# Optimization experiments

Measured on AMD Instinct MI355X. Metric: run time of the kernel, lower is better.

## Reference

```python
import jax, jax.numpy as jnp
import numpy as np

N_NODES = 100000
N_EDGES = 1600000


def setup_inputs() -> dict:
    key = jax.random.key(0)
    k1, k2, k3, k4, k5, k6 = jax.random.split(key, 6)
    x = jax.random.normal(k1, (N_NODES, 2), dtype=jnp.float32)
    edge_index = jax.random.randint(k2, (2, N_EDGES), 0, N_NODES, dtype=jnp.int64)
    # Glorot-style init for GCN weights, zeros for biases (PyG defaults)
    W1 = jax.random.normal(k3, (2, 64), dtype=jnp.float32) * (1.0 / np.sqrt(2.0))
    b1 = jnp.zeros((64,), dtype=jnp.float32)
    W2 = jax.random.normal(k4, (64, 1), dtype=jnp.float32) * (1.0 / np.sqrt(64.0))
    b2 = jnp.zeros((1,), dtype=jnp.float32)
    return {"x": x, "edge_index": edge_index, "W1": W1, "b1": b1, "W2": W2, "b2": b2}


def reference(x, edge_index, W1, b1, W2, b2):
    N = x.shape[0]
    row, col = edge_index[0], edge_index[1]  # source, target (PyG flow source_to_target)
    # symmetric GCN normalization, degrees from target index (no self loops)
    deg = jax.ops.segment_sum(jnp.ones(edge_index.shape[1], x.dtype), col, num_segments=N)
    deg_inv_sqrt = jnp.where(deg > 0, jnp.where(deg > 0, deg, 1.0) ** -0.5, 0.0)
    norm = (deg_inv_sqrt[row] * deg_inv_sqrt[col])[:, None]  # [E,1]

    def gcn_conv(h, W, b):
        h = h @ W                       # [N,F_out] tiny GEMM
        msg = h[row] * norm             # gather + scale: [E,F_out]
        agg = jax.ops.segment_sum(msg, col, num_segments=N)  # scatter-add
        return agg + b

    h = jax.nn.relu(gcn_conv(x, W1, b1))   # dropout is identity in eval mode
    out = jax.nn.relu(gcn_conv(h, W2, b2))
    return out
```

## Files before the change

### kernel.cpp

```cpp
#include <hip/hip_runtime.h>
#include <math.h>

#define NN 100000
#define NE 1600000
#define BKT 448
#define NB 224
#define EPB 6400
#define NPB 250
#define STRIDE 8192
#define RT 1024

__global__ void __launch_bounds__(RT) reorder_kernel(
        const int* __restrict__ row, const int* __restrict__ col,
        unsigned* __restrict__ cursor, unsigned* __restrict__ packed) {
    __shared__ int h[NB], lb[NB];
    __shared__ unsigned gaddr[NB], glim[NB];
    __shared__ int wsum[RT / 64];
    __shared__ uint2 sga[EPB];
    const int t = threadIdx.x;
    const int lane = t & 63, wid = t >> 6;
    const int e0 = blockIdx.x * EPB;

    for (int i = t; i < NB; i += RT) h[i] = 0;
    __syncthreads();

    const int4* rv = (const int4*)(row + e0);
    const int4* cv = (const int4*)(col + e0);
    unsigned pk[8]; int bb[8];
#pragma unroll
    for (int u = 0; u < 8; ++u) bb[u] = -1;
#pragma unroll
    for (int g = 0; g < 2; ++g) {
        int grp = g * RT + t;
        if (grp < EPB / 4) {
            int4 r4 = rv[grp], c4 = cv[grp];
            int rr[4] = {r4.x, r4.y, r4.z, r4.w};
            int cc[4] = {c4.x, c4.y, c4.z, c4.w};
#pragma unroll
            for (int j = 0; j < 4; ++j) {
                int b = cc[j] / BKT;
                int cl = cc[j] - b * BKT;
                pk[4 * g + j] = ((unsigned)rr[j] << 9) | (unsigned)cl;
                bb[4 * g + j] = b;
            }
        }
    }
#pragma unroll
    for (int u = 0; u < 8; ++u)
        if (bb[u] >= 0) atomicAdd(&h[bb[u]], 1);
    __syncthreads();

    int v = (t < NB) ? h[t] : 0;
    int incl = v;
#pragma unroll
    for (int d = 1; d < 64; d <<= 1) {
        int u2 = __shfl_up(incl, d);
        if (lane >= d) incl += u2;
    }
    if (lane == 63) wsum[wid] = incl;
    __syncthreads();
    int off = 0;
#pragma unroll
    for (int j = 0; j < 3; ++j)
        if (j < wid) off += wsum[j];
    if (t < NB) {
        lb[t] = off + incl - v;
        unsigned base = v ? atomicAdd(&cursor[t], (unsigned)v) : 0u;
        gaddr[t] = (unsigned)t * STRIDE + base;
        glim[t]  = (unsigned)(t + 1) * STRIDE;
    }
    __syncthreads();
    for (int i = t; i < NB; i += RT) h[i] = 0;
    __syncthreads();

#pragma unroll
    for (int u = 0; u < 8; ++u) {
        if (bb[u] >= 0) {
            int b = bb[u];
            int r = atomicAdd(&h[b], 1);
            unsigned a = gaddr[b] + (unsigned)r;
            if (a >= glim[b]) a = 0xFFFFFFFFu;
            sga[lb[b] + r] = make_uint2(pk[u], a);
        }
    }
    __syncthreads();
    for (int i = t; i < EPB; i += RT) {
        uint2 e = sga[i];
        if (e.y != 0xFFFFFFFFu) packed[e.y] = e.x;
    }
}

__global__ void __launch_bounds__(RT) sortb_kernel(
        const unsigned* __restrict__ packed, const unsigned* __restrict__ cursor,
        const float2* __restrict__ x2,
        unsigned* __restrict__ srow, int2* __restrict__ node_rng,
        float* __restrict__ dis, float2* __restrict__ y2) {
    __shared__ int cnt[BKT], rk[BKT], sexA[BKT];
    __shared__ int wsum[(BKT + 63) / 64];
    __shared__ unsigned srt[STRIDE];
    const int t = threadIdx.x;
    const int lane = t & 63, wid = t >> 6;
    const int b = blockIdx.x;
    const unsigned s0 = (unsigned)b * STRIDE;
    const int L = min((int)cursor[b], STRIDE);
    const int L4 = L >> 2;

    for (int i = t; i < BKT; i += RT) { cnt[i] = 0; rk[i] = 0; }
    __syncthreads();

    const uint4* pv4 = (const uint4*)(packed + s0);
    for (int g = t; g < L4; g += RT) {
        uint4 p4 = pv4[g];
        atomicAdd(&cnt[p4.x & 511u], 1);
        atomicAdd(&cnt[p4.y & 511u], 1);
        atomicAdd(&cnt[p4.z & 511u], 1);
        atomicAdd(&cnt[p4.w & 511u], 1);
    }
    for (int i = 4 * L4 + t; i < L; i += RT)
        atomicAdd(&cnt[packed[s0 + i] & 511u], 1);
    __syncthreads();

    int v = (t < BKT) ? cnt[t] : 0;
    int incl = v;
#pragma unroll
    for (int d = 1; d < 64; d <<= 1) {
        int u2 = __shfl_up(incl, d);
        if (lane >= d) incl += u2;
    }
    if (lane == 63 && wid < (BKT + 63) / 64) wsum[wid] = incl;
    __syncthreads();
    int off = 0;
#pragma unroll
    for (int j = 0; j < (BKT + 63) / 64 - 1; ++j)
        if (j < wid) off += wsum[j];
    if (t < BKT) {
        int sex = off + incl - v;
        sexA[t] = sex;
        int node = b * BKT + t;
        if (node < NN) {
            float dv = (v > 0) ? rsqrtf((float)v) : 0.0f;
            dis[node] = dv;
            float2 xv = x2[node];
            y2[node] = make_float2(xv.x * dv, xv.y * dv);
            node_rng[node] = make_int2((int)(s0 + sex), (int)(s0 + sex + v));
        }
    }
    __syncthreads();

    for (int g = t; g < L4; g += RT) {
        uint4 p4 = pv4[g];
        unsigned pp[4] = {p4.x, p4.y, p4.z, p4.w};
#pragma unroll
        for (int j = 0; j < 4; ++j) {
            int cl = pp[j] & 511u;
            int r = atomicAdd(&rk[cl], 1);
            srt[sexA[cl] + r] = pp[j] >> 9;
        }
    }
    for (int i = 4 * L4 + t; i < L; i += RT) {
        unsigned p = packed[s0 + i];
        int cl = p & 511u;
        int r = atomicAdd(&rk[cl], 1);
        srt[sexA[cl] + r] = p >> 9;
    }
    __syncthreads();
    uint4* so4 = (uint4*)(srow + s0);
    for (int g = t; g < L4; g += RT) so4[g] = ((const uint4*)srt)[g];
    for (int i = 4 * L4 + t; i < L; i += RT) srow[s0 + i] = srt[i];
}

__global__ void conv1_kernel(const unsigned* __restrict__ srow, const int2* __restrict__ node_rng,
                             const float2* __restrict__ y2, const float* __restrict__ dis,
                             const float* __restrict__ W1, const float* __restrict__ b1,
                             const float* __restrict__ W2, float* __restrict__ z2) {
    __shared__ float sW0[64], sW1[64], sb1[64], sW2[64];
    int t = threadIdx.x;
    if (t < 64) { sW0[t] = W1[t]; sW1[t] = W1[64 + t]; sb1[t] = b1[t]; sW2[t] = W2[t]; }
    __syncthreads();
    int lane = t & 3;
    int node = blockIdx.x * 64 + (t >> 2);
    if (node >= NN) return;
    int2 rng = node_rng[node];
    float sx = 0.f, sy = 0.f;
    for (int k = rng.x + lane; k < rng.y; k += 4) {
        float2 v = y2[srow[k]];
        sx += v.x; sy += v.y;
    }
    sx += __shfl_xor(sx, 1); sy += __shfl_xor(sy, 1);
    sx += __shfl_xor(sx, 2); sy += __shfl_xor(sy, 2);
    float dv = dis[node];
    float a0 = sx * dv, a1 = sy * dv;
    float acc = 0.0f;
    int j0 = lane * 16;
#pragma unroll
    for (int jj = 0; jj < 16; ++jj) {
        int j = j0 + jj;
        float h = fmaf(a0, sW0[j], fmaf(a1, sW1[j], sb1[j]));
        acc = fmaf(fmaxf(h, 0.0f), sW2[j], acc);
    }
    acc += __shfl_xor(acc, 1);
    acc += __shfl_xor(acc, 2);
    if (lane == 0) z2[node] = acc * dv;
}

__global__ void conv2_kernel(const unsigned* __restrict__ srow, const int2* __restrict__ node_rng,
                             const float* __restrict__ z2, const float* __restrict__ dis,
                             const float* __restrict__ b2, float* __restrict__ out) {
    int t = threadIdx.x;
    int lane = t & 3;
    int node = blockIdx.x * 64 + (t >> 2);
    if (node >= NN) return;
    int2 rng = node_rng[node];
    float s = 0.f;
    for (int k = rng.x + lane; k < rng.y; k += 4)
        s += z2[srow[k]];
    s += __shfl_xor(s, 1);
    s += __shfl_xor(s, 2);
    if (lane == 0)
        out[node] = fmaxf(fmaf(dis[node], s, b2[0]), 0.0f);
}

extern "C" void kernel_launch(void* const* d_in, const int* in_sizes, int n_in,
                              void* d_out, int out_size, void* d_ws, size_t ws_size,
                              hipStream_t stream) {
    const float* x  = (const float*)d_in[0];
    const int*   ei = (const int*)d_in[1];
    const float* W1 = (const float*)d_in[2];
    const float* b1 = (const float*)d_in[3];
    const float* W2 = (const float*)d_in[4];
    const float* b2 = (const float*)d_in[5];
    float* out = (float*)d_out;

    const int* row = ei;
    const int* col = ei + NE;

    unsigned* packed   = (unsigned*)d_ws;
    unsigned* srow     = packed + (size_t)NB * STRIDE;
    float2*   y2       = (float2*)(srow + (size_t)NB * STRIDE);
    float*    dis      = (float*)(y2 + NN);
    float*    z2       = dis + NN;
    int2*     node_rng = (int2*)(z2 + NN);
    unsigned* cursor   = (unsigned*)(node_rng + NN);

    hipMemsetAsync(cursor, 0, NB * sizeof(unsigned), stream);

    reorder_kernel<<<NPB, RT, 0, stream>>>(row, col, cursor, packed);
    sortb_kernel  <<<NB, RT, 0, stream>>>(packed, cursor, (const float2*)x,
                                          srow, node_rng, dis, y2);
    conv1_kernel  <<<(NN + 63) / 64, 256, 0, stream>>>(srow, node_rng, y2, dis,
                                                       W1, b1, W2, z2);
    conv2_kernel  <<<(NN + 63) / 64, 256, 0, stream>>>(srow, node_rng, z2, dis, b2, out);
}
```

Before: 113.0 us.

## Replace per-bucket counting sort with LDS atomic accumulation in conv kernels

```diff
diff --git a/kernel.cpp b/kernel.cpp
--- a/kernel.cpp
+++ b/kernel.cpp
@@ -90,22 +90,18 @@
     }
 }
 
-__global__ void __launch_bounds__(RT) sortb_kernel(
+__global__ void __launch_bounds__(RT) degree_kernel(
         const unsigned* __restrict__ packed, const unsigned* __restrict__ cursor,
         const float2* __restrict__ x2,
-        unsigned* __restrict__ srow, int2* __restrict__ node_rng,
         float* __restrict__ dis, float2* __restrict__ y2) {
-    __shared__ int cnt[BKT], rk[BKT], sexA[BKT];
-    __shared__ int wsum[(BKT + 63) / 64];
-    __shared__ unsigned srt[STRIDE];
-    const int t = threadIdx.x;
-    const int lane = t & 63, wid = t >> 6;
+    __shared__ int cnt[BKT];
+    const int t = threadIdx.x;
     const int b = blockIdx.x;
     const unsigned s0 = (unsigned)b * STRIDE;
     const int L = min((int)cursor[b], STRIDE);
     const int L4 = L >> 2;
 
-    for (int i = t; i < BKT; i += RT) { cnt[i] = 0; rk[i] = 0; }
+    for (int i = t; i < BKT; i += RT) cnt[i] = 0;
     __syncthreads();
 
     const uint4* pv4 = (const uint4*)(packed + s0);
@@ -120,104 +116,104 @@
         atomicAdd(&cnt[packed[s0 + i] & 511u], 1);
     __syncthreads();
 
-    int v = (t < BKT) ? cnt[t] : 0;
-    int incl = v;
-#pragma unroll
-    for (int d = 1; d < 64; d <<= 1) {
-        int u2 = __shfl_up(incl, d);
-        if (lane >= d) incl += u2;
-    }
-    if (lane == 63 && wid < (BKT + 63) / 64) wsum[wid] = incl;
-    __syncthreads();
-    int off = 0;
-#pragma unroll
-    for (int j = 0; j < (BKT + 63) / 64 - 1; ++j)
-        if (j < wid) off += wsum[j];
-    if (t < BKT) {
-        int sex = off + incl - v;
-        sexA[t] = sex;
-        int node = b * BKT + t;
-        if (node < NN) {
-            float dv = (v > 0) ? rsqrtf((float)v) : 0.0f;
-            dis[node] = dv;
-            float2 xv = x2[node];
-            y2[node] = make_float2(xv.x * dv, xv.y * dv);
-            node_rng[node] = make_int2((int)(s0 + sex), (int)(s0 + sex + v));
-        }
-    }
-    __syncthreads();
-
+    int node = b * BKT + t;
+    if (t < BKT && node < NN) {
+        int v = cnt[t];
+        float dv = (v > 0) ? rsqrtf((float)v) : 0.0f;
+        dis[node] = dv;
+        float2 xv = x2[node];
+        y2[node] = make_float2(xv.x * dv, xv.y * dv);
+    }
+}
+
+__global__ void __launch_bounds__(RT) conv1_kernel(
+        const unsigned* __restrict__ packed, const unsigned* __restrict__ cursor,
+        const float2* __restrict__ y2, const float* __restrict__ dis,
+        const float* __restrict__ W1, const float* __restrict__ b1,
+        const float* __restrict__ W2, float* __restrict__ z2) {
+    __shared__ float accx[BKT], accy[BKT];
+    __shared__ float sW0[64], sW1[64], sb1[64], sW2[64];
+    const int t = threadIdx.x;
+    const int b = blockIdx.x;
+    const unsigned s0 = (unsigned)b * STRIDE;
+    const int L = min((int)cursor[b], STRIDE);
+    const int L4 = L >> 2;
+
+    if (t < 64) { sW0[t] = W1[t]; sW1[t] = W1[64 + t]; sb1[t] = b1[t]; sW2[t] = W2[t]; }
+    for (int i = t; i < BKT; i += RT) { accx[i] = 0.0f; accy[i] = 0.0f; }
+    __syncthreads();
+
+    const uint4* pv4 = (const uint4*)(packed + s0);
     for (int g = t; g < L4; g += RT) {
         uint4 p4 = pv4[g];
         unsigned pp[4] = {p4.x, p4.y, p4.z, p4.w};
+        float2 vv[4];
+#pragma unroll
+        for (int j = 0; j < 4; ++j) vv[j] = y2[pp[j] >> 9];
 #pragma unroll
         for (int j = 0; j < 4; ++j) {
             int cl = pp[j] & 511u;
-            int r = atomicAdd(&rk[cl], 1);
-            srt[sexA[cl] + r] = pp[j] >> 9;
+            atomicAdd(&accx[cl], vv[j].x);
+            atomicAdd(&accy[cl], vv[j].y);
         }
     }
     for (int i = 4 * L4 + t; i < L; i += RT) {
         unsigned p = packed[s0 + i];
+        float2 v = y2[p >> 9];
         int cl = p & 511u;
-        int r = atomicAdd(&rk[cl], 1);
-        srt[sexA[cl] + r] = p >> 9;
-    }
-    __syncthreads();
-    uint4* so4 = (uint4*)(srow + s0);
-    for (int g = t; g < L4; g += RT) so4[g] = ((const uint4*)srt)[g];
-    for (int i = 4 * L4 + t; i < L; i += RT) srow[s0 + i] = srt[i];
-}
-
-__global__ void conv1_kernel(const unsigned* __restrict__ srow, const int2* __restrict__ node_rng,
-                             const float2* __restrict__ y2, const float* __restrict__ dis,
-                             const float* __restrict__ W1, const float* __restrict__ b1,
-                             const float* __restrict__ W2, float* __restrict__ z2) {
-    __shared__ float sW0[64], sW1[64], sb1[64], sW2[64];
-    int t = threadIdx.x;
-    if (t < 64) { sW0[t] = W1[t]; sW1[t] = W1[64 + t]; sb1[t] = b1[t]; sW2[t] = W2[t]; }
-    __syncthreads();
-    int lane = t & 3;
-    int node = blockIdx.x * 64 + (t >> 2);
-    if (node >= NN) return;
-    int2 rng = node_rng[node];
-    float sx = 0.f, sy = 0.f;
-    for (int k = rng.x + lane; k < rng.y; k += 4) {
-        float2 v = y2[srow[k]];
-        sx += v.x; sy += v.y;
-    }
-    sx += __shfl_xor(sx, 1); sy += __shfl_xor(sy, 1);
-    sx += __shfl_xor(sx, 2); sy += __shfl_xor(sy, 2);
-    float dv = dis[node];
-    float a0 = sx * dv, a1 = sy * dv;
-    float acc = 0.0f;
-    int j0 = lane * 16;
-#pragma unroll
-    for (int jj = 0; jj < 16; ++jj) {
-        int j = j0 + jj;
-        float h = fmaf(a0, sW0[j], fmaf(a1, sW1[j], sb1[j]));
-        acc = fmaf(fmaxf(h, 0.0f), sW2[j], acc);
-    }
-    acc += __shfl_xor(acc, 1);
-    acc += __shfl_xor(acc, 2);
-    if (lane == 0) z2[node] = acc * dv;
-}
-
-__global__ void conv2_kernel(const unsigned* __restrict__ srow, const int2* __restrict__ node_rng,
-                             const float* __restrict__ z2, const float* __restrict__ dis,
-                             const float* __restrict__ b2, float* __restrict__ out) {
-    int t = threadIdx.x;
-    int lane = t & 3;
-    int node = blockIdx.x * 64 + (t >> 2);
-    if (node >= NN) return;
-    int2 rng = node_rng[node];
-    float s = 0.f;
-    for (int k = rng.x + lane; k < rng.y; k += 4)
-        s += z2[srow[k]];
-    s += __shfl_xor(s, 1);
-    s += __shfl_xor(s, 2);
-    if (lane == 0)
-        out[node] = fmaxf(fmaf(dis[node], s, b2[0]), 0.0f);
+        atomicAdd(&accx[cl], v.x);
+        atomicAdd(&accy[cl], v.y);
+    }
+    __syncthreads();
+
+    int node = b * BKT + t;
+    if (t < BKT && node < NN) {
+        float dv = dis[node];
+        float a0 = accx[t] * dv, a1 = accy[t] * dv;
+        float acc = 0.0f;
+#pragma unroll
+        for (int j = 0; j < 64; ++j) {
+            float h = fmaf(a0, sW0[j], fmaf(a1, sW1[j], sb1[j]));
+            acc = fmaf(fmaxf(h, 0.0f), sW2[j], acc);
+        }
+        z2[node] = acc * dv;
+    }
+}
+
+__global__ void __launch_bounds__(RT) conv2_kernel(
+        const unsigned* __restrict__ packed, const unsigned* __restrict__ cursor,
+        const float* __restrict__ z2, const float* __restrict__ dis,
+        const float* __restrict__ b2, float* __restrict__ out) {
+    __shared__ float acc[BKT];
+    const int t = threadIdx.x;
+    const int b = blockIdx.x;
+    const unsigned s0 = (unsigned)b * STRIDE;
+    const int L = min((int)cursor[b], STRIDE);
+    const int L4 = L >> 2;
+
+    for (int i = t; i < BKT; i += RT) acc[i] = 0.0f;
+    __syncthreads();
+
+    const uint4* pv4 = (const uint4*)(packed + s0);
+    for (int g = t; g < L4; g += RT) {
+        uint4 p4 = pv4[g];
+        unsigned pp[4] = {p4.x, p4.y, p4.z, p4.w};
+        float vv[4];
+#pragma unroll
+        for (int j = 0; j < 4; ++j) vv[j] = z2[pp[j] >> 9];
+#pragma unroll
+        for (int j = 0; j < 4; ++j)
+            atomicAdd(&acc[pp[j] & 511u], vv[j]);
+    }
+    for (int i = 4 * L4 + t; i < L; i += RT) {
+        unsigned p = packed[s0 + i];
+        atomicAdd(&acc[p & 511u], z2[p >> 9]);
+    }
+    __syncthreads();
+
+    int node = b * BKT + t;
+    if (t < BKT && node < NN)
+        out[node] = fmaxf(fmaf(dis[node], acc[t], b2[0]), 0.0f);
 }
 
 extern "C" void kernel_launch(void* const* d_in, const int* in_sizes, int n_in,
@@ -235,19 +231,15 @@
     const int* col = ei + NE;
 
     unsigned* packed   = (unsigned*)d_ws;
-    unsigned* srow     = packed + (size_t)NB * STRIDE;
-    float2*   y2       = (float2*)(srow + (size_t)NB * STRIDE);
+    float2*   y2       = (float2*)(packed + (size_t)NB * STRIDE);
     float*    dis      = (float*)(y2 + NN);
     float*    z2       = dis + NN;
-    int2*     node_rng = (int2*)(z2 + NN);
-    unsigned* cursor   = (unsigned*)(node_rng + NN);
+    unsigned* cursor   = (unsigned*)(z2 + NN);
 
     hipMemsetAsync(cursor, 0, NB * sizeof(unsigned), stream);
 
     reorder_kernel<<<NPB, RT, 0, stream>>>(row, col, cursor, packed);
-    sortb_kernel  <<<NB, RT, 0, stream>>>(packed, cursor, (const float2*)x,
-                                          srow, node_rng, dis, y2);
-    conv1_kernel  <<<(NN + 63) / 64, 256, 0, stream>>>(srow, node_rng, y2, dis,
-                                                       W1, b1, W2, z2);
-    conv2_kernel  <<<(NN + 63) / 64, 256, 0, stream>>>(srow, node_rng, z2, dis, b2, out);
-}
+    degree_kernel <<<NB, RT, 0, stream>>>(packed, cursor, (const float2*)x, dis, y2);
+    conv1_kernel  <<<NB, RT, 0, stream>>>(packed, cursor, y2, dis, W1, b1, W2, z2);
+    conv2_kernel  <<<NB, RT, 0, stream>>>(packed, cursor, z2, dis, b2, out);
+}
```

New measurement: 120.1 us. 6.3% more time.

## Fuse bucket sort and both GCN convolutions into one cooperative kernel

Applied to the files above, without the earlier changes.

```diff
diff --git a/kernel.cpp b/kernel.cpp
--- a/kernel.cpp
+++ b/kernel.cpp
@@ -1,5 +1,8 @@
 #include <hip/hip_runtime.h>
+#include <hip/hip_cooperative_groups.h>
 #include <math.h>
+
+namespace cg = cooperative_groups;
 
 #define NN 100000
 #define NE 1600000
@@ -90,14 +93,18 @@
     }
 }
 
-__global__ void __launch_bounds__(RT) sortb_kernel(
+__global__ void __launch_bounds__(RT) fused_kernel(
         const unsigned* __restrict__ packed, const unsigned* __restrict__ cursor,
         const float2* __restrict__ x2,
-        unsigned* __restrict__ srow, int2* __restrict__ node_rng,
-        float* __restrict__ dis, float2* __restrict__ y2) {
+        const float* __restrict__ W1, const float* __restrict__ b1,
+        const float* __restrict__ W2, const float* __restrict__ b2,
+        float2* __restrict__ y2, float* __restrict__ z2, float* __restrict__ out) {
     __shared__ int cnt[BKT], rk[BKT], sexA[BKT];
     __shared__ int wsum[(BKT + 63) / 64];
+    __shared__ float sW0[64], sW1[64], sb1[64], sW2[64];
     __shared__ unsigned srt[STRIDE];
+    cg::grid_group grid = cg::this_grid();
+
     const int t = threadIdx.x;
     const int lane = t & 63, wid = t >> 6;
     const int b = blockIdx.x;
@@ -105,6 +112,7 @@
     const int L = min((int)cursor[b], STRIDE);
     const int L4 = L >> 2;
 
+    if (t < 64) { sW0[t] = W1[t]; sW1[t] = W1[64 + t]; sb1[t] = b1[t]; sW2[t] = W2[t]; }
     for (int i = t; i < BKT; i += RT) { cnt[i] = 0; rk[i] = 0; }
     __syncthreads();
 
@@ -134,18 +142,16 @@
     for (int j = 0; j < (BKT + 63) / 64 - 1; ++j)
         if (j < wid) off += wsum[j];
     if (t < BKT) {
-        int sex = off + incl - v;
-        sexA[t] = sex;
+        sexA[t] = off + incl - v;
         int node = b * BKT + t;
         if (node < NN) {
             float dv = (v > 0) ? rsqrtf((float)v) : 0.0f;
-            dis[node] = dv;
             float2 xv = x2[node];
             y2[node] = make_float2(xv.x * dv, xv.y * dv);
-            node_rng[node] = make_int2((int)(s0 + sex), (int)(s0 + sex + v));
-        }
-    }
-    __syncthreads();
+        }
+    }
+    __threadfence();
+    grid.sync();
 
     for (int g = t; g < L4; g += RT) {
         uint4 p4 = pv4[g];
@@ -164,60 +170,45 @@
         srt[sexA[cl] + r] = p >> 9;
     }
     __syncthreads();
-    uint4* so4 = (uint4*)(srow + s0);
-    for (int g = t; g < L4; g += RT) so4[g] = ((const uint4*)srt)[g];
-    for (int i = 4 * L4 + t; i < L; i += RT) srow[s0 + i] = srt[i];
-}
-
-__global__ void conv1_kernel(const unsigned* __restrict__ srow, const int2* __restrict__ node_rng,
-                             const float2* __restrict__ y2, const float* __restrict__ dis,
-                             const float* __restrict__ W1, const float* __restrict__ b1,
-                             const float* __restrict__ W2, float* __restrict__ z2) {
-    __shared__ float sW0[64], sW1[64], sb1[64], sW2[64];
-    int t = threadIdx.x;
-    if (t < 64) { sW0[t] = W1[t]; sW1[t] = W1[64 + t]; sb1[t] = b1[t]; sW2[t] = W2[t]; }
-    __syncthreads();
-    int lane = t & 3;
-    int node = blockIdx.x * 64 + (t >> 2);
-    if (node >= NN) return;
-    int2 rng = node_rng[node];
-    float sx = 0.f, sy = 0.f;
-    for (int k = rng.x + lane; k < rng.y; k += 4) {
-        float2 v = y2[srow[k]];
-        sx += v.x; sy += v.y;
-    }
-    sx += __shfl_xor(sx, 1); sy += __shfl_xor(sy, 1);
-    sx += __shfl_xor(sx, 2); sy += __shfl_xor(sy, 2);
-    float dv = dis[node];
-    float a0 = sx * dv, a1 = sy * dv;
-    float acc = 0.0f;
-    int j0 = lane * 16;
-#pragma unroll
-    for (int jj = 0; jj < 16; ++jj) {
-        int j = j0 + jj;
-        float h = fmaf(a0, sW0[j], fmaf(a1, sW1[j], sb1[j]));
-        acc = fmaf(fmaxf(h, 0.0f), sW2[j], acc);
-    }
-    acc += __shfl_xor(acc, 1);
-    acc += __shfl_xor(acc, 2);
-    if (lane == 0) z2[node] = acc * dv;
-}
-
-__global__ void conv2_kernel(const unsigned* __restrict__ srow, const int2* __restrict__ node_rng,
-                             const float* __restrict__ z2, const float* __restrict__ dis,
-                             const float* __restrict__ b2, float* __restrict__ out) {
-    int t = threadIdx.x;
-    int lane = t & 3;
-    int node = blockIdx.x * 64 + (t >> 2);
-    if (node >= NN) return;
-    int2 rng = node_rng[node];
-    float s = 0.f;
-    for (int k = rng.x + lane; k < rng.y; k += 4)
-        s += z2[srow[k]];
-    s += __shfl_xor(s, 1);
-    s += __shfl_xor(s, 2);
-    if (lane == 0)
-        out[node] = fmaxf(fmaf(dis[node], s, b2[0]), 0.0f);
+
+    const int tau = t >> 1, par = t & 1;
+    if (t < 2 * BKT) {
+        int start = sexA[tau], deg = cnt[tau];
+        float sx = 0.f, sy = 0.f;
+        for (int k = start + par; k < start + deg; k += 2) {
+            float2 w = y2[srt[k]];
+            sx += w.x; sy += w.y;
+        }
+        sx += __shfl_xor(sx, 1); sy += __shfl_xor(sy, 1);
+        float dv = (deg > 0) ? rsqrtf((float)deg) : 0.0f;
+        float a0 = sx * dv, a1 = sy * dv;
+        float acc = 0.0f;
+        int j0 = par * 32;
+#pragma unroll
+        for (int jj = 0; jj < 32; ++jj) {
+            int j = j0 + jj;
+            float h = fmaf(a0, sW0[j], fmaf(a1, sW1[j], sb1[j]));
+            acc = fmaf(fmaxf(h, 0.0f), sW2[j], acc);
+        }
+        acc += __shfl_xor(acc, 1);
+        int node = b * BKT + tau;
+        if (par == 0 && node < NN) z2[node] = acc * dv;
+    }
+    __threadfence();
+    grid.sync();
+
+    if (t < 2 * BKT) {
+        int start = sexA[tau], deg = cnt[tau];
+        float s = 0.f;
+        for (int k = start + par; k < start + deg; k += 2)
+            s += z2[srt[k]];
+        s += __shfl_xor(s, 1);
+        int node = b * BKT + tau;
+        if (par == 0 && node < NN) {
+            float dv = (deg > 0) ? rsqrtf((float)deg) : 0.0f;
+            out[node] = fmaxf(fmaf(dv, s, b2[0]), 0.0f);
+        }
+    }
 }
 
 extern "C" void kernel_launch(void* const* d_in, const int* in_sizes, int n_in,
@@ -234,20 +225,18 @@
     const int* row = ei;
     const int* col = ei + NE;
 
-    unsigned* packed   = (unsigned*)d_ws;
-    unsigned* srow     = packed + (size_t)NB * STRIDE;
-    float2*   y2       = (float2*)(srow + (size_t)NB * STRIDE);
-    float*    dis      = (float*)(y2 + NN);
-    float*    z2       = dis + NN;
-    int2*     node_rng = (int2*)(z2 + NN);
-    unsigned* cursor   = (unsigned*)(node_rng + NN);
+    unsigned* packed = (unsigned*)d_ws;
+    float2*   y2     = (float2*)(packed + (size_t)NB * STRIDE);
+    float*    z2     = (float*)(y2 + NN);
+    unsigned* cursor = (unsigned*)(z2 + NN);
 
     hipMemsetAsync(cursor, 0, NB * sizeof(unsigned), stream);
 
     reorder_kernel<<<NPB, RT, 0, stream>>>(row, col, cursor, packed);
-    sortb_kernel  <<<NB, RT, 0, stream>>>(packed, cursor, (const float2*)x,
-                                          srow, node_rng, dis, y2);
-    conv1_kernel  <<<(NN + 63) / 64, 256, 0, stream>>>(srow, node_rng, y2, dis,
-                                                       W1, b1, W2, z2);
-    conv2_kernel  <<<(NN + 63) / 64, 256, 0, stream>>>(srow, node_rng, z2, dis, b2, out);
+
+    void* args[] = {(void*)&packed, (void*)&cursor, (void*)&x,
+                    (void*)&W1, (void*)&b1, (void*)&W2, (void*)&b2,
+                    (void*)&y2, (void*)&z2, (void*)&out};
+    hipLaunchCooperativeKernel((void*)fused_kernel, dim3(NB), dim3(RT),
+                               args, 0, stream);
 }
```

New measurement: 282.3 us. 2.5x slower.

## Split degree pass and fuse bucket sort with first GCN aggregation

Applied to the files above, without the earlier changes.

```diff
diff --git a/kernel.cpp b/kernel.cpp
--- a/kernel.cpp
+++ b/kernel.cpp
@@ -90,13 +90,52 @@
     }
 }
 
-__global__ void __launch_bounds__(RT) sortb_kernel(
+__global__ void __launch_bounds__(RT) degree_kernel(
         const unsigned* __restrict__ packed, const unsigned* __restrict__ cursor,
         const float2* __restrict__ x2,
+        float* __restrict__ dis, float2* __restrict__ y2) {
+    __shared__ int cnt[BKT];
+    const int t = threadIdx.x;
+    const int b = blockIdx.x;
+    const unsigned s0 = (unsigned)b * STRIDE;
+    const int L = min((int)cursor[b], STRIDE);
+    const int L4 = L >> 2;
+
+    for (int i = t; i < BKT; i += RT) cnt[i] = 0;
+    __syncthreads();
+
+    const uint4* pv4 = (const uint4*)(packed + s0);
+    for (int g = t; g < L4; g += RT) {
+        uint4 p4 = pv4[g];
+        atomicAdd(&cnt[p4.x & 511u], 1);
+        atomicAdd(&cnt[p4.y & 511u], 1);
+        atomicAdd(&cnt[p4.z & 511u], 1);
+        atomicAdd(&cnt[p4.w & 511u], 1);
+    }
+    for (int i = 4 * L4 + t; i < L; i += RT)
+        atomicAdd(&cnt[packed[s0 + i] & 511u], 1);
+    __syncthreads();
+
+    int node = b * BKT + t;
+    if (t < BKT && node < NN) {
+        int v = cnt[t];
+        float dv = (v > 0) ? rsqrtf((float)v) : 0.0f;
+        dis[node] = dv;
+        float2 xv = x2[node];
+        y2[node] = make_float2(xv.x * dv, xv.y * dv);
+    }
+}
+
+__global__ void __launch_bounds__(RT) sortconv1_kernel(
+        const unsigned* __restrict__ packed, const unsigned* __restrict__ cursor,
+        const float2* __restrict__ y2,
+        const float* __restrict__ W1, const float* __restrict__ b1,
+        const float* __restrict__ W2,
         unsigned* __restrict__ srow, int2* __restrict__ node_rng,
-        float* __restrict__ dis, float2* __restrict__ y2) {
+        float* __restrict__ z2) {
     __shared__ int cnt[BKT], rk[BKT], sexA[BKT];
     __shared__ int wsum[(BKT + 63) / 64];
+    __shared__ float sW0[64], sW1[64], sb1[64], sW2[64];
     __shared__ unsigned srt[STRIDE];
     const int t = threadIdx.x;
     const int lane = t & 63, wid = t >> 6;
@@ -105,6 +144,7 @@
     const int L = min((int)cursor[b], STRIDE);
     const int L4 = L >> 2;
 
+    if (t < 64) { sW0[t] = W1[t]; sW1[t] = W1[64 + t]; sb1[t] = b1[t]; sW2[t] = W2[t]; }
     for (int i = t; i < BKT; i += RT) { cnt[i] = 0; rk[i] = 0; }
     __syncthreads();
 
@@ -137,13 +177,8 @@
         int sex = off + incl - v;
         sexA[t] = sex;
         int node = b * BKT + t;
-        if (node < NN) {
-            float dv = (v > 0) ? rsqrtf((float)v) : 0.0f;
-            dis[node] = dv;
-            float2 xv = x2[node];
-            y2[node] = make_float2(xv.x * dv, xv.y * dv);
+        if (node < NN)
             node_rng[node] = make_int2((int)(s0 + sex), (int)(s0 + sex + v));
-        }
     }
     __syncthreads();
 
@@ -164,43 +199,34 @@
         srt[sexA[cl] + r] = p >> 9;
     }
     __syncthreads();
+
     uint4* so4 = (uint4*)(srow + s0);
     for (int g = t; g < L4; g += RT) so4[g] = ((const uint4*)srt)[g];
     for (int i = 4 * L4 + t; i < L; i += RT) srow[s0 + i] = srt[i];
-}
-
-__global__ void conv1_kernel(const unsigned* __restrict__ srow, const int2* __restrict__ node_rng,
-                             const float2* __restrict__ y2, const float* __restrict__ dis,
-                             const float* __restrict__ W1, const float* __restrict__ b1,
-                             const float* __restrict__ W2, float* __restrict__ z2) {
-    __shared__ float sW0[64], sW1[64], sb1[64], sW2[64];
-    int t = threadIdx.x;
-    if (t < 64) { sW0[t] = W1[t]; sW1[t] = W1[64 + t]; sb1[t] = b1[t]; sW2[t] = W2[t]; }
-    __syncthreads();
-    int lane = t & 3;
-    int node = blockIdx.x * 64 + (t >> 2);
-    if (node >= NN) return;
-    int2 rng = node_rng[node];
-    float sx = 0.f, sy = 0.f;
-    for (int k = rng.x + lane; k < rng.y; k += 4) {
-        float2 v = y2[srow[k]];
-        sx += v.x; sy += v.y;
-    }
-    sx += __shfl_xor(sx, 1); sy += __shfl_xor(sy, 1);
-    sx += __shfl_xor(sx, 2); sy += __shfl_xor(sy, 2);
-    float dv = dis[node];
-    float a0 = sx * dv, a1 = sy * dv;
-    float acc = 0.0f;
-    int j0 = lane * 16;
-#pragma unroll
-    for (int jj = 0; jj < 16; ++jj) {
-        int j = j0 + jj;
-        float h = fmaf(a0, sW0[j], fmaf(a1, sW1[j], sb1[j]));
-        acc = fmaf(fmaxf(h, 0.0f), sW2[j], acc);
-    }
-    acc += __shfl_xor(acc, 1);
-    acc += __shfl_xor(acc, 2);
-    if (lane == 0) z2[node] = acc * dv;
+
+    const int tau = t >> 1, par = t & 1;
+    if (t < 2 * BKT) {
+        int start = sexA[tau], deg = cnt[tau];
+        float sx = 0.f, sy = 0.f;
+        for (int k = start + par; k < start + deg; k += 2) {
+            float2 w = y2[srt[k]];
+            sx += w.x; sy += w.y;
+        }
+        sx += __shfl_xor(sx, 1); sy += __shfl_xor(sy, 1);
+        float dv = (deg > 0) ? rsqrtf((float)deg) : 0.0f;
+        float a0 = sx * dv, a1 = sy * dv;
+        float acc = 0.0f;
+        int j0 = par * 32;
+#pragma unroll
+        for (int jj = 0; jj < 32; ++jj) {
+            int j = j0 + jj;
+            float h = fmaf(a0, sW0[j], fmaf(a1, sW1[j], sb1[j]));
+            acc = fmaf(fmaxf(h, 0.0f), sW2[j], acc);
+        }
+        acc += __shfl_xor(acc, 1);
+        int node = b * BKT + tau;
+        if (par == 0 && node < NN) z2[node] = acc * dv;
+    }
 }
 
 __global__ void conv2_kernel(const unsigned* __restrict__ srow, const int2* __restrict__ node_rng,
@@ -244,10 +270,9 @@
 
     hipMemsetAsync(cursor, 0, NB * sizeof(unsigned), stream);
 
-    reorder_kernel<<<NPB, RT, 0, stream>>>(row, col, cursor, packed);
-    sortb_kernel  <<<NB, RT, 0, stream>>>(packed, cursor, (const float2*)x,
-                                          srow, node_rng, dis, y2);
-    conv1_kernel  <<<(NN + 63) / 64, 256, 0, stream>>>(srow, node_rng, y2, dis,
-                                                       W1, b1, W2, z2);
-    conv2_kernel  <<<(NN + 63) / 64, 256, 0, stream>>>(srow, node_rng, z2, dis, b2, out);
-}
+    reorder_kernel  <<<NPB, RT, 0, stream>>>(row, col, cursor, packed);
+    degree_kernel   <<<NB, RT, 0, stream>>>(packed, cursor, (const float2*)x, dis, y2);
+    sortconv1_kernel<<<NB, RT, 0, stream>>>(packed, cursor, (const float2*)y2,
+                                            W1, b1, W2, srow, node_rng, z2);
+    conv2_kernel    <<<(NN + 63) / 64, 256, 0, stream>>>(srow, node_rng, z2, dis, b2, out);
+}
```

After: 111.3 us. Within noise of the previous version (-1.5%).
